# Kernel optimization log

Hardware: AMD Instinct MI355X
Metric: run time of the kernel (lower is better)

## Reference

```python
import jax, jax.numpy as jnp
import numpy as np

# Static per-expert capacities (tokens are laid out contiguously per expert)
CAPS = [1024, 512, 1024, 256, 1024, 512, 128, 1024, 512, 1024, 256, 512, 1024, 128, 64, 512]
TOTAL = sum(CAPS)  # 9536
E, H, I = 16, 1024, 4096
OFFSETS = np.concatenate([[0], np.cumsum(CAPS)])


def setup_inputs() -> dict:
    key = jax.random.key(0)
    ks = jax.random.split(key, 5)
    x = jax.random.normal(ks[0], (TOTAL, H), dtype=jnp.float32)
    W1 = jax.random.normal(ks[1], (E, I, H), dtype=jnp.float32) * 0.02
    b1 = jax.random.normal(ks[2], (E, I), dtype=jnp.float32) * 0.02
    W2 = jax.random.normal(ks[3], (E, H, I), dtype=jnp.float32) * 0.02
    b2 = jax.random.normal(ks[4], (E, H), dtype=jnp.float32) * 0.02
    return {"x": x, "W1": W1, "b1": b1, "W2": W2, "b2": b2}


def reference(x, W1, b1, W2, b2):
    # Grouped GEMM FFN: expert e processes rows [OFFSETS[e]:OFFSETS[e+1]]
    # out = gelu(x_e @ W1[e].T + b1[e]) @ W2[e].T + b2[e]
    outs = []
    for e in range(E):  # fixed, static loop over experts (capacities are static)
        xs = x[OFFSETS[e]:OFFSETS[e + 1]]                      # [cap_e, H]
        h = jax.nn.gelu(xs @ W1[e].T + b1[e], approximate=False)  # [cap_e, I]
        outs.append(h @ W2[e].T + b2[e])                       # [cap_e, H]
    return jnp.concatenate(outs, axis=0)                       # [TOTAL, H]
```

## Files before the change

### kernel.cpp

```cpp
#include <hip/hip_runtime.h>
#include <math.h>

typedef __attribute__((ext_vector_type(8))) short short8;
typedef __attribute__((ext_vector_type(4))) float f32x4;
typedef __attribute__((ext_vector_type(2))) unsigned int u32x2;
typedef __attribute__((ext_vector_type(4))) unsigned int u32x4;

#define E_NUM 16
constexpr int CAPS[E_NUM] = {1024,512,1024,256,1024,512,128,1024,512,1024,256,512,1024,128,64,512};
constexpr int OFFS[E_NUM] = {0,1024,1536,2560,2816,3840,4352,4480,5504,6016,7040,7296,7808,8832,8960,9024};
constexpr int cdiv_(int a, int b){ return (a + b - 1) / b; }
constexpr int ilog2_(int v){ int l = 0; while ((1 << l) < v) ++l; return l; }

__device__ __forceinline__ unsigned int cvt_pk_bf16(float a, float b){
  unsigned int r;
  asm("v_cvt_pk_bf16_f32 %0, %1, %2" : "=v"(r) : "v"(a), "v"(b));
  return r;
}

typedef __attribute__((address_space(1))) const unsigned char gas_u8;
typedef __attribute__((address_space(3))) unsigned char las_u8;
__device__ __forceinline__ void gl_lds16(const void* g, void* l){
  __builtin_amdgcn_global_load_lds((gas_u8*)g, (las_u8*)l, 16, 0, 0);
}

__global__ __launch_bounds__(256) void cvt_bf16_kernel(const float* __restrict__ x,
                                                       unsigned short* __restrict__ xb, int n8)
{
  int i = blockIdx.x * blockDim.x + threadIdx.x;
  const int stride = gridDim.x * blockDim.x;
  for (; i < n8; i += stride) {
    f32x4 a = *reinterpret_cast<const f32x4*>(x + (size_t)i * 8);
    f32x4 b = *reinterpret_cast<const f32x4*>(x + (size_t)i * 8 + 4);
    u32x2 lo, hi;
    lo[0] = cvt_pk_bf16(a[0], a[1]); lo[1] = cvt_pk_bf16(a[2], a[3]);
    hi[0] = cvt_pk_bf16(b[0], b[1]); hi[1] = cvt_pk_bf16(b[2], b[3]);
    *reinterpret_cast<u32x2*>(xb + (size_t)i * 8)     = lo;
    *reinterpret_cast<u32x2*>(xb + (size_t)i * 8 + 4) = hi;
  }
}

template<bool A_BF16, int NDIM, int KDIM, int LOG_GN, int NWG>
__global__ __launch_bounds__(512, 2)
void g1_gemm256(const void* __restrict__ Av, const float* __restrict__ W,
                const float* __restrict__ bias, void* __restrict__ Outv)
{
  constexpr int A_BYTES = 256 * 64;
  constexpr int B_BYTES = 256 * 128;
  constexpr int BUF  = A_BYTES + B_BYTES;
  constexpr int NBUF = A_BF16 ? 3 : 2;
  constexpr int GN   = 1 << LOG_GN;
  constexpr int NTT  = KDIM / 32;
  static_assert(NWG % 8 == 0);
  static_assert(NTT >= 3);

  __shared__ __align__(16) char smem[NBUF * BUF];

  const int tid  = threadIdx.x;
  const int braw = blockIdx.x;
  const int tt = (braw & 7) * (NWG / 8) + (braw >> 3);

  int m0 = 0, n0 = 0, Me = 0, tok0 = 0;
  size_t wbase = 0, bbase = 0;
  {
    int acc0 = 0;
    #pragma unroll
    for (int i = 0; i < E_NUM; ++i) {
      const int mt  = cdiv_(CAPS[i], 256);
      const int lmt = ilog2_(mt);
      const int nb  = mt * (NDIM / 256);
      if (tt >= acc0 && tt < acc0 + nb) {
        const int loc = tt - acc0;
        const int g   = loc >> (lmt + LOG_GN);
        const int rem = loc & ((mt << LOG_GN) - 1);
        m0   = (rem >> LOG_GN) * 256;
        n0   = ((g << LOG_GN) | (rem & (GN - 1))) * 256;
        Me   = CAPS[i];
        tok0 = OFFS[i];
        wbase = (size_t)i * NDIM * KDIM;
        bbase = (size_t)i * NDIM;
      }
      acc0 += nb;
    }
  }
  const float* Wb = W + wbase;

  const int lane = tid & 63;
  const int wv   = tid >> 6;

  const unsigned short* Ah = (const unsigned short*)Av;
  const float*          Af = (const float*)Av;

  auto stageA = [&](int buf, int kt) {
    const unsigned short* Ag = Ah + (size_t)(tok0 + m0) * KDIM + kt * 32;
    char* dst0 = smem + buf * BUF;
    #pragma unroll
    for (int j = 0; j < 2; ++j) {
      const int rbase = j * 128 + wv * 16;
      const int r     = rbase + (lane >> 2);
      const int blk   = (lane & 3) ^ (r & 3);
      gl_lds16((const void*)(Ag + (size_t)r * KDIM + blk * 8), (void*)(dst0 + rbase * 64));
    }
  };
  auto stageB = [&](int buf, int kt) {
    const float* Bg = Wb + (size_t)n0 * KDIM + kt * 32;
    char* dst0 = smem + buf * BUF + A_BYTES;
    #pragma unroll
    for (int j = 0; j < 4; ++j) {
      const int rbase = j * 64 + wv * 8;
      const int r     = rbase + (lane >> 3);
      const int blk   = (lane & 7) ^ (r & 7);
      gl_lds16((const void*)(Bg + (size_t)r * KDIM + blk * 4), (void*)(dst0 + rbase * 128));
    }
  };

  const int fr = tid >> 1;
  const int fcq = (tid & 1) * 2;
  f32x4 raf[4];
  auto loadA_reg = [&](int kt) {
    const float* Ap = Af + (size_t)(tok0 + m0 + fr) * KDIM + kt * 32 + fcq * 8;
    #pragma unroll
    for (int i = 0; i < 4; ++i) raf[i] = *reinterpret_cast<const f32x4*>(Ap + i * 4);
  };
  auto writeA_reg = [&](int buf) {
    char* ab = smem + buf * BUF;
    #pragma unroll
    for (int i = 0; i < 2; ++i) {
      u32x2 p;
      p[0] = cvt_pk_bf16(raf[2*i][0], raf[2*i][1]);
      p[1] = cvt_pk_bf16(raf[2*i][2], raf[2*i][3]);
      const int blk = (fcq + i) ^ (fr & 3);
      *reinterpret_cast<u32x2*>(ab + fr * 64 + blk * 16) = p;
    }
  };

  const int wm   = (wv >> 2) * 128;
  const int wn   = (wv & 3) * 64;
  const int lrow = lane & 15;
  const int pa0  = (((lane >> 4) ^ (lane & 3)) << 4);
  const int pb0  = ((((lane >> 4) << 1) ^ (lane & 7)) << 4);

  f32x4 acc_[8][4];
  #pragma unroll
  for (int i = 0; i < 8; ++i)
    #pragma unroll
    for (int j = 0; j < 4; ++j)
      acc_[i][j] = (f32x4){0.f, 0.f, 0.f, 0.f};

  auto compute = [&](int cur) {
    const char* ab  = smem + cur * BUF;
    const char* bbp = smem + cur * BUF + A_BYTES;
    short8 bfr[4];
    #pragma unroll
    for (int f = 0; f < 4; ++f) {
      const char* rowp = bbp + (size_t)(wn + f * 16 + lrow) * 128;
      f32x4 lo = *reinterpret_cast<const f32x4*>(rowp + pb0);
      f32x4 hi = *reinterpret_cast<const f32x4*>(rowp + (pb0 ^ 16));
      u32x4 pk;
      pk[0] = cvt_pk_bf16(lo[0], lo[1]); pk[1] = cvt_pk_bf16(lo[2], lo[3]);
      pk[2] = cvt_pk_bf16(hi[0], hi[1]); pk[3] = cvt_pk_bf16(hi[2], hi[3]);
      bfr[f] = __builtin_bit_cast(short8, pk);
    }
    #pragma unroll
    for (int i = 0; i < 8; ++i) {
      short8 afr = *reinterpret_cast<const short8*>(ab + (wm + i * 16 + lrow) * 64 + pa0);
      #pragma unroll
      for (int j = 0; j < 4; ++j)
        acc_[i][j] = __builtin_amdgcn_mfma_f32_16x16x32_bf16(afr, bfr[j], acc_[i][j], 0, 0, 0);
    }
  };

  if constexpr (A_BF16) {
    stageA(0, 0); stageB(0, 0);
    stageA(1, 1); stageB(1, 1);
    int cur = 0, nx2 = 2;
    for (int kt = 0; kt < NTT; ++kt) {
      if (kt + 1 < NTT) asm volatile("s_waitcnt vmcnt(6)\n\ts_barrier" ::: "memory");
      else              asm volatile("s_waitcnt vmcnt(0)\n\ts_barrier" ::: "memory");
      __builtin_amdgcn_sched_barrier(0);
      if (kt + 2 < NTT) { stageA(nx2, kt + 2); stageB(nx2, kt + 2); }
      compute(cur);
      cur = (cur == 2) ? 0 : cur + 1;
      nx2 = (nx2 == 2) ? 0 : nx2 + 1;
    }
  } else {
    loadA_reg(0); stageB(0, 0); writeA_reg(0);
    __syncthreads();
    for (int kt = 0; kt < NTT; ++kt) {
      const int cur = kt & 1;
      if (kt + 1 < NTT) { stageB(cur ^ 1, kt + 1); loadA_reg(kt + 1); }
      compute(cur);
      if (kt + 1 < NTT) writeA_reg(cur ^ 1);
      __syncthreads();
    }
  }

  float bv[4];
  #pragma unroll
  for (int f = 0; f < 4; ++f)
    bv[f] = bias[bbase + n0 + wn + f * 16 + lrow];

  unsigned short* Oh = (unsigned short*)Outv;
  if constexpr (A_BF16) {
    __syncthreads();
    unsigned short* hout = (unsigned short*)smem;
    #pragma unroll
    for (int i = 0; i < 8; ++i) {
      const int rbase = wm + i * 16 + (lane >> 4) * 4;
      #pragma unroll
      for (int j = 0; j < 4; ++j) {
        #pragma unroll
        for (int jj = 0; jj < 4; ++jj) {
          float xv = acc_[i][j][jj] + bv[j];
          float y2 = xv * (1.5957691216057308f + 0.07135481627f * xv * xv);
          float g  = xv * __builtin_amdgcn_rcpf(1.0f + __expf(-y2));
          hout[(rbase + jj) * 256 + wn + j * 16 + lrow] = (unsigned short)(cvt_pk_bf16(g, g) & 0xFFFFu);
        }
      }
    }
    __syncthreads();
    #pragma unroll
    for (int s = 0; s < 16; ++s) {
      const int row = s * 16 + (tid >> 5);
      const int c   = (tid & 31) * 8;
      if (m0 + row < Me) {
        *reinterpret_cast<short8*>(Oh + (size_t)(tok0 + m0 + row) * NDIM + n0 + c)
          = *reinterpret_cast<const short8*>(hout + row * 256 + c);
      }
    }
  } else {
    #pragma unroll
    for (int i = 0; i < 8; ++i) {
      const int rbase = wm + i * 16 + (lane >> 4) * 4;
      #pragma unroll
      for (int j = 0; j < 4; ++j) {
        #pragma unroll
        for (int jj = 0; jj < 4; ++jj) {
          int grow = m0 + rbase + jj;
          if (grow < Me) {
            float xv = acc_[i][j][jj] + bv[j];
            float y2 = xv * (1.5957691216057308f + 0.07135481627f * xv * xv);
            float g  = xv * __builtin_amdgcn_rcpf(1.0f + __expf(-y2));
            Oh[(size_t)(tok0 + grow) * NDIM + n0 + wn + j * 16 + lrow]
              = (unsigned short)(cvt_pk_bf16(g, g) & 0xFFFFu);
          }
        }
      }
    }
  }
}

template<int NDIM, int KDIM, int LOG_GN, int NWG, int KS>
__global__ __launch_bounds__(256, 4)
void g2_gemm128(const unsigned short* __restrict__ Ah, const float* __restrict__ W,
                const float* __restrict__ bias, float* __restrict__ Of)
{
  constexpr int A_BYTES = 128 * 64;
  constexpr int B_BYTES = 128 * 128;
  constexpr int BUF  = A_BYTES + B_BYTES;
  constexpr int GN   = 1 << LOG_GN;
  constexpr int NT   = KDIM / (KS * 32);
  constexpr int NWG1 = NWG / KS;
  static_assert(NWG % 8 == 0);
  static_assert(NT >= 3);

  __shared__ __align__(16) char smem[3 * BUF];

  const int tid  = threadIdx.x;
  const int braw = blockIdx.x;
  const int t = (braw & 7) * (NWG / 8) + (braw >> 3);

  const int kc    = t / NWG1;
  const int tt    = t % NWG1;
  const int kbase = kc * (KDIM / KS);

  int m0 = 0, n0 = 0, Me = 0, tok0 = 0;
  size_t wbase = 0, bbase = 0;
  {
    int acc0 = 0;
    #pragma unroll
    for (int i = 0; i < E_NUM; ++i) {
      const int mt  = cdiv_(CAPS[i], 128);
      const int lmt = ilog2_(mt);
      const int nb  = mt * (NDIM / 128);
      if (tt >= acc0 && tt < acc0 + nb) {
        const int loc = tt - acc0;
        const int g   = loc >> (lmt + LOG_GN);
        const int rem = loc & ((mt << LOG_GN) - 1);
        m0   = (rem >> LOG_GN) * 128;
        n0   = ((g << LOG_GN) | (rem & (GN - 1))) * 128;
        Me   = CAPS[i];
        tok0 = OFFS[i];
        wbase = (size_t)i * NDIM * KDIM;
        bbase = (size_t)i * NDIM;
      }
      acc0 += nb;
    }
  }
  const float* Wb = W + wbase;

  const int lane = tid & 63;
  const int wv   = tid >> 6;

  auto stageA = [&](int buf, int kt) {
    const unsigned short* Ag = Ah + (size_t)(tok0 + m0) * KDIM + kbase + kt * 32;
    char* dst0 = smem + buf * BUF;
    #pragma unroll
    for (int j = 0; j < 2; ++j) {
      const int rbase = j * 64 + wv * 16;
      const int r     = rbase + (lane >> 2);
      const int blk   = (lane & 3) ^ (r & 3);
      gl_lds16((const void*)(Ag + (size_t)r * KDIM + blk * 8), (void*)(dst0 + rbase * 64));
    }
  };
  auto stageB = [&](int buf, int kt) {
    const float* Bg = Wb + (size_t)n0 * KDIM + kbase + kt * 32;
    char* dst0 = smem + buf * BUF + A_BYTES;
    #pragma unroll
    for (int j = 0; j < 4; ++j) {
      const int rbase = j * 32 + wv * 8;
      const int r     = rbase + (lane >> 3);
      const int blk   = (lane & 7) ^ (r & 7);
      gl_lds16((const void*)(Bg + (size_t)r * KDIM + blk * 4), (void*)(dst0 + rbase * 128));
    }
  };

  const int wm   = (wv >> 1) * 64;
  const int wn   = (wv & 1) * 64;
  const int lrow = lane & 15;
  const int pa0  = (((lane >> 4) ^ (lane & 3)) << 4);
  const int pb0  = ((((lane >> 4) << 1) ^ (lane & 7)) << 4);

  f32x4 acc_[4][4];
  #pragma unroll
  for (int i = 0; i < 4; ++i)
    #pragma unroll
    for (int j = 0; j < 4; ++j)
      acc_[i][j] = (f32x4){0.f, 0.f, 0.f, 0.f};

  auto compute = [&](int cur) {
    const char* ab  = smem + cur * BUF;
    const char* bbp = smem + cur * BUF + A_BYTES;
    short8 bfr[4];
    #pragma unroll
    for (int f = 0; f < 4; ++f) {
      const char* rowp = bbp + (size_t)(wn + f * 16 + lrow) * 128;
      f32x4 lo = *reinterpret_cast<const f32x4*>(rowp + pb0);
      f32x4 hi = *reinterpret_cast<const f32x4*>(rowp + (pb0 ^ 16));
      u32x4 pk;
      pk[0] = cvt_pk_bf16(lo[0], lo[1]); pk[1] = cvt_pk_bf16(lo[2], lo[3]);
      pk[2] = cvt_pk_bf16(hi[0], hi[1]); pk[3] = cvt_pk_bf16(hi[2], hi[3]);
      bfr[f] = __builtin_bit_cast(short8, pk);
    }
    #pragma unroll
    for (int i = 0; i < 4; ++i) {
      short8 afr = *reinterpret_cast<const short8*>(ab + (wm + i * 16 + lrow) * 64 + pa0);
      #pragma unroll
      for (int j = 0; j < 4; ++j)
        acc_[i][j] = __builtin_amdgcn_mfma_f32_16x16x32_bf16(afr, bfr[j], acc_[i][j], 0, 0, 0);
    }
  };

  stageA(0, 0); stageB(0, 0);
  stageA(1, 1); stageB(1, 1);
  int cur = 0, nx2 = 2;
  for (int kt = 0; kt < NT; ++kt) {
    if (kt + 1 < NT) asm volatile("s_waitcnt vmcnt(6)\n\ts_barrier" ::: "memory");
    else             asm volatile("s_waitcnt vmcnt(0)\n\ts_barrier" ::: "memory");
    __builtin_amdgcn_sched_barrier(0);
    if (kt + 2 < NT) { stageA(nx2, kt + 2); stageB(nx2, kt + 2); }
    compute(cur);
    cur = (cur == 2) ? 0 : cur + 1;
    nx2 = (nx2 == 2) ? 0 : nx2 + 1;
  }

  float bv[4];
  #pragma unroll
  for (int f = 0; f < 4; ++f)
    bv[f] = bias[bbase + n0 + wn + f * 16 + lrow];

  constexpr float BS = 1.0f / (float)KS;
  #pragma unroll
  for (int i = 0; i < 4; ++i) {
    const int rbase = wm + i * 16 + (lane >> 4) * 4;
    #pragma unroll
    for (int jj = 0; jj < 4; ++jj) {
      int grow = m0 + rbase + jj;
      if (grow < Me) {
        #pragma unroll
        for (int j = 0; j < 4; ++j) {
          float v = acc_[i][j][jj] + bv[j] * BS;
          float* p = Of + (size_t)(tok0 + grow) * NDIM + n0 + wn + j * 16 + lrow;
          if constexpr (KS > 1) unsafeAtomicAdd(p, v);
          else                  *p = v;
        }
      }
    }
  }
}

extern "C" void kernel_launch(void* const* d_in, const int* in_sizes, int n_in,
                              void* d_out, int out_size, void* d_ws, size_t ws_size,
                              hipStream_t stream)
{
  const float* x  = (const float*)d_in[0];
  const float* W1 = (const float*)d_in[1];
  const float* b1 = (const float*)d_in[2];
  const float* W2 = (const float*)d_in[3];
  const float* b2 = (const float*)d_in[4];
  float* out = (float*)d_out;

  constexpr size_t H_BYTES  = (size_t)9536 * 4096 * 2;
  constexpr size_t XB_BYTES = (size_t)9536 * 1024 * 2;
  unsigned short* h  = (unsigned short*)d_ws;
  unsigned short* xb = (unsigned short*)((char*)d_ws + H_BYTES);

  const bool use_xb = ws_size >= H_BYTES + XB_BYTES;

  hipMemsetAsync(d_out, 0, (size_t)out_size * sizeof(float), stream);

  if (use_xb) {
    cvt_bf16_kernel<<<2048, 256, 0, stream>>>(x, xb, 9536 * 1024 / 8);
    g1_gemm256<true, 4096, 1024, 2, 624>
        <<<624, 512, 0, stream>>>((const void*)xb, W1, b1, (void*)h);
  } else {
    g1_gemm256<false, 4096, 1024, 2, 624>
        <<<624, 512, 0, stream>>>((const void*)x, W1, b1, (void*)h);
  }

  g2_gemm128<1024, 4096, 2, 1200, 2>
      <<<1200, 256, 0, stream>>>(h, W2, b2, out);
}
```

Before: 364.4 us.

## Retile second GEMM to 256x256 with register-staged bf16 weight conversion

Replaces the 128x128 second-stage GEMM with a 256x256 tile using 512 threads and split-K of 4. The fp32 W2 tiles are now loaded into registers, converted to bf16 once, and written to LDS, so they are no longer converted repeatedly inside the MFMA loop. The K loop is restructured into a 6-phase unrolled pipeline with triple-buffered A and double-buffered B. The aim is higher arithmetic intensity and less LDS traffic. In exchange, register pressure rises and the larger split-K means more atomic adds to the output.

Measured after the change: 456.5 us. 25.3% more time.

```diff
diff --git a/kernel.cpp b/kernel.cpp
--- a/kernel.cpp
+++ b/kernel.cpp
@@ -250,26 +250,25 @@
   }
 }
 
-template<int NDIM, int KDIM, int LOG_GN, int NWG, int KS>
-__global__ __launch_bounds__(256, 4)
-void g2_gemm128(const unsigned short* __restrict__ Ah, const float* __restrict__ W,
+template<int NDIM, int KDIM, int NWG, int KS>
+__global__ __launch_bounds__(512, 2)
+void g2_gemm256(const unsigned short* __restrict__ Ah, const float* __restrict__ W,
                 const float* __restrict__ bias, float* __restrict__ Of)
 {
-  constexpr int A_BYTES = 128 * 64;
-  constexpr int B_BYTES = 128 * 128;
-  constexpr int BUF  = A_BYTES + B_BYTES;
-  constexpr int GN   = 1 << LOG_GN;
+  constexpr int A_BYTES = 256 * 64;
+  constexpr int B_BYTES = 256 * 64;
   constexpr int NT   = KDIM / (KS * 32);
   constexpr int NWG1 = NWG / KS;
   static_assert(NWG % 8 == 0);
-  static_assert(NT >= 3);
-
-  __shared__ __align__(16) char smem[3 * BUF];
+  static_assert(NT >= 6 && (NT % 6 == 2), "loop is 6-phase unrolled + 2 tail iters");
+
+  __shared__ __align__(16) char smem[3 * A_BYTES + 2 * B_BYTES];
+  char* abuf = smem;
+  char* bbuf = smem + 3 * A_BYTES;
 
   const int tid  = threadIdx.x;
   const int braw = blockIdx.x;
   const int t = (braw & 7) * (NWG / 8) + (braw >> 3);
-
   const int kc    = t / NWG1;
   const int tt    = t % NWG1;
   const int kbase = kc * (KDIM / KS);
@@ -280,15 +279,12 @@
     int acc0 = 0;
     #pragma unroll
     for (int i = 0; i < E_NUM; ++i) {
-      const int mt  = cdiv_(CAPS[i], 128);
-      const int lmt = ilog2_(mt);
-      const int nb  = mt * (NDIM / 128);
+      const int mt = cdiv_(CAPS[i], 256);
+      const int nb = mt * (NDIM / 256);
       if (tt >= acc0 && tt < acc0 + nb) {
         const int loc = tt - acc0;
-        const int g   = loc >> (lmt + LOG_GN);
-        const int rem = loc & ((mt << LOG_GN) - 1);
-        m0   = (rem >> LOG_GN) * 128;
-        n0   = ((g << LOG_GN) | (rem & (GN - 1))) * 128;
+        m0   = (loc & (mt - 1)) * 256;
+        n0   = (loc >> ilog2_(mt)) * 256;
         Me   = CAPS[i];
         tok0 = OFFS[i];
         wbase = (size_t)i * NDIM * KDIM;
@@ -302,58 +298,57 @@
   const int lane = tid & 63;
   const int wv   = tid >> 6;
 
-  auto stageA = [&](int buf, int kt) {
+  auto stageA = [&](char* dst0, int kt) {
     const unsigned short* Ag = Ah + (size_t)(tok0 + m0) * KDIM + kbase + kt * 32;
-    char* dst0 = smem + buf * BUF;
     #pragma unroll
     for (int j = 0; j < 2; ++j) {
-      const int rbase = j * 64 + wv * 16;
+      const int rbase = wv * 32 + j * 16;
       const int r     = rbase + (lane >> 2);
       const int blk   = (lane & 3) ^ (r & 3);
       gl_lds16((const void*)(Ag + (size_t)r * KDIM + blk * 8), (void*)(dst0 + rbase * 64));
     }
   };
-  auto stageB = [&](int buf, int kt) {
-    const float* Bg = Wb + (size_t)n0 * KDIM + kbase + kt * 32;
-    char* dst0 = smem + buf * BUF + A_BYTES;
-    #pragma unroll
-    for (int j = 0; j < 4; ++j) {
-      const int rbase = j * 32 + wv * 8;
-      const int r     = rbase + (lane >> 3);
-      const int blk   = (lane & 7) ^ (r & 7);
-      gl_lds16((const void*)(Bg + (size_t)r * KDIM + blk * 4), (void*)(dst0 + rbase * 128));
-    }
-  };
-
-  const int wm   = (wv >> 1) * 64;
-  const int wn   = (wv & 1) * 64;
+
+  const int br  = tid >> 1;
+  const int bkh = (tid & 1) * 16;
+  auto loadB = [&](f32x4 (&R)[4], int kt) {
+    const float* p = Wb + (size_t)(n0 + br) * KDIM + kbase + kt * 32 + bkh;
+    #pragma unroll
+    for (int i = 0; i < 4; ++i) R[i] = *reinterpret_cast<const f32x4*>(p + i * 4);
+  };
+  auto writeB = [&](char* dst0, f32x4 (&R)[4]) {
+    const int s = (br >> 1) & 3;
+    u32x4 q0, q1;
+    q0[0] = cvt_pk_bf16(R[0][0], R[0][1]); q0[1] = cvt_pk_bf16(R[0][2], R[0][3]);
+    q0[2] = cvt_pk_bf16(R[1][0], R[1][1]); q0[3] = cvt_pk_bf16(R[1][2], R[1][3]);
+    q1[0] = cvt_pk_bf16(R[2][0], R[2][1]); q1[1] = cvt_pk_bf16(R[2][2], R[2][3]);
+    q1[2] = cvt_pk_bf16(R[3][0], R[3][1]); q1[3] = cvt_pk_bf16(R[3][2], R[3][3]);
+    const int b0 = (((tid & 1) * 2) + 0) ^ s;
+    const int b1 = (((tid & 1) * 2) + 1) ^ s;
+    *reinterpret_cast<u32x4*>(dst0 + br * 64 + b0 * 16) = q0;
+    *reinterpret_cast<u32x4*>(dst0 + br * 64 + b1 * 16) = q1;
+  };
+
+  const int wm   = (wv >> 2) * 128;
+  const int wn   = (wv & 3) * 64;
   const int lrow = lane & 15;
   const int pa0  = (((lane >> 4) ^ (lane & 3)) << 4);
-  const int pb0  = ((((lane >> 4) << 1) ^ (lane & 7)) << 4);
-
-  f32x4 acc_[4][4];
+  const int pb0  = (((lane >> 4) ^ ((lane >> 1) & 3)) << 4);
+
+  f32x4 acc_[8][4];
   #pragma unroll
-  for (int i = 0; i < 4; ++i)
+  for (int i = 0; i < 8; ++i)
     #pragma unroll
     for (int j = 0; j < 4; ++j)
       acc_[i][j] = (f32x4){0.f, 0.f, 0.f, 0.f};
 
-  auto compute = [&](int cur) {
-    const char* ab  = smem + cur * BUF;
-    const char* bbp = smem + cur * BUF + A_BYTES;
+  auto compute = [&](const char* ab, const char* bb) {
     short8 bfr[4];
     #pragma unroll
-    for (int f = 0; f < 4; ++f) {
-      const char* rowp = bbp + (size_t)(wn + f * 16 + lrow) * 128;
-      f32x4 lo = *reinterpret_cast<const f32x4*>(rowp + pb0);
-      f32x4 hi = *reinterpret_cast<const f32x4*>(rowp + (pb0 ^ 16));
-      u32x4 pk;
-      pk[0] = cvt_pk_bf16(lo[0], lo[1]); pk[1] = cvt_pk_bf16(lo[2], lo[3]);
-      pk[2] = cvt_pk_bf16(hi[0], hi[1]); pk[3] = cvt_pk_bf16(hi[2], hi[3]);
-      bfr[f] = __builtin_bit_cast(short8, pk);
-    }
-    #pragma unroll
-    for (int i = 0; i < 4; ++i) {
+    for (int f = 0; f < 4; ++f)
+      bfr[f] = *reinterpret_cast<const short8*>(bb + (wn + f * 16 + lrow) * 64 + pb0);
+    #pragma unroll
+    for (int i = 0; i < 8; ++i) {
       short8 afr = *reinterpret_cast<const short8*>(ab + (wm + i * 16 + lrow) * 64 + pa0);
       #pragma unroll
       for (int j = 0; j < 4; ++j)
@@ -361,18 +356,35 @@
     }
   };
 
-  stageA(0, 0); stageB(0, 0);
-  stageA(1, 1); stageB(1, 1);
-  int cur = 0, nx2 = 2;
-  for (int kt = 0; kt < NT; ++kt) {
-    if (kt + 1 < NT) asm volatile("s_waitcnt vmcnt(6)\n\ts_barrier" ::: "memory");
-    else             asm volatile("s_waitcnt vmcnt(0)\n\ts_barrier" ::: "memory");
-    __builtin_amdgcn_sched_barrier(0);
-    if (kt + 2 < NT) { stageA(nx2, kt + 2); stageB(nx2, kt + 2); }
-    compute(cur);
-    cur = (cur == 2) ? 0 : cur + 1;
-    nx2 = (nx2 == 2) ? 0 : nx2 + 1;
-  }
+  f32x4 Br0[4], Br1[4], Br2[4];
+  loadB(Br0, 0); loadB(Br1, 1);
+  stageA(abuf + 0 * A_BYTES, 0);
+  stageA(abuf + 1 * A_BYTES, 1);
+  loadB(Br2, 2);
+  asm volatile("s_waitcnt vmcnt(12)" ::: "memory");
+  writeB(bbuf + 0 * B_BYTES, Br0);
+
+#define G2_ITER(T, AC, AS, BC, BW, BRW, BRL)                                        \
+  { const int t_ = (T);                                                             \
+    if (t_ + 3 <= NT) { asm volatile("s_waitcnt vmcnt(6) lgkmcnt(0)\n\ts_barrier" ::: "memory"); } \
+    else              { asm volatile("s_waitcnt vmcnt(0) lgkmcnt(0)\n\ts_barrier" ::: "memory"); } \
+    __builtin_amdgcn_sched_barrier(0);                                              \
+    if (t_ + 1 < NT) writeB(bbuf + (BW) * B_BYTES, BRW);                            \
+    if (t_ + 3 < NT) loadB(BRL, t_ + 3);                                            \
+    if (t_ + 2 < NT) stageA(abuf + (AS) * A_BYTES, t_ + 2);                         \
+    compute(abuf + (AC) * A_BYTES, bbuf + (BC) * B_BYTES); }
+
+  for (int tb = 0; tb < NT - 2; tb += 6) {
+    G2_ITER(tb + 0, 0, 2, 0, 1, Br1, Br0)
+    G2_ITER(tb + 1, 1, 0, 1, 0, Br2, Br1)
+    G2_ITER(tb + 2, 2, 1, 0, 1, Br0, Br2)
+    G2_ITER(tb + 3, 0, 2, 1, 0, Br1, Br0)
+    G2_ITER(tb + 4, 1, 0, 0, 1, Br2, Br1)
+    G2_ITER(tb + 5, 2, 1, 1, 0, Br0, Br2)
+  }
+  G2_ITER(NT - 2, 0, 2, 0, 1, Br1, Br0)
+  G2_ITER(NT - 1, 1, 0, 1, 0, Br2, Br1)
+#undef G2_ITER
 
   float bv[4];
   #pragma unroll
@@ -381,7 +393,7 @@
 
   constexpr float BS = 1.0f / (float)KS;
   #pragma unroll
-  for (int i = 0; i < 4; ++i) {
+  for (int i = 0; i < 8; ++i) {
     const int rbase = wm + i * 16 + (lane >> 4) * 4;
     #pragma unroll
     for (int jj = 0; jj < 4; ++jj) {
@@ -390,9 +402,7 @@
         #pragma unroll
         for (int j = 0; j < 4; ++j) {
           float v = acc_[i][j][jj] + bv[j] * BS;
-          float* p = Of + (size_t)(tok0 + grow) * NDIM + n0 + wn + j * 16 + lrow;
-          if constexpr (KS > 1) unsafeAtomicAdd(p, v);
-          else                  *p = v;
+          unsafeAtomicAdd(Of + (size_t)(tok0 + grow) * NDIM + n0 + wn + j * 16 + lrow, v);
         }
       }
     }
@@ -428,6 +438,6 @@
         <<<624, 512, 0, stream>>>((const void*)x, W1, b1, (void*)h);
   }
 
-  g2_gemm128<1024, 4096, 2, 1200, 2>
-      <<<1200, 256, 0, stream>>>(h, W2, b2, out);
-}
+  g2_gemm256<1024, 4096, 624, 4>
+      <<<624, 512, 0, stream>>>(h, W2, b2, out);
+}
```
